# Optimization experiments

Hardware: AMD Instinct MI355X
Metric: run time of the kernel (lower is better)

The kernel has to match this reference:

```python
import jax, jax.numpy as jnp
import numpy as np

N = 16384  # cohort size; original kernel materializes an N x N tril matrix (1 GB fp32)


def setup_inputs() -> dict:
    key = jax.random.key(0)
    k1, k2, k3 = jax.random.split(key, 3)
    pred = jax.random.normal(k1, (N, 1), dtype=jnp.float32)
    # survival times sorted in DESCENDING order (docstring precondition)
    ytime = jnp.sort(jax.random.uniform(k2, (N, 1), dtype=jnp.float32), axis=0)[::-1]
    # binary censoring/event indicator, ~half observed
    yevent = (jax.random.uniform(k3, (N, 1), dtype=jnp.float32) < 0.5).astype(jnp.float32)
    label = jnp.concatenate([ytime, yevent], axis=1)  # [N, 2]
    return {"pred": pred, "label": label}


def reference(pred, label):
    # yevent: [N,1] event indicator (label[:,1]); ytime only fixes ordering/length.
    yevent = label[:, 1:2]
    n_observed = yevent.sum()
    # tril(ones) @ exp(pred) is exactly an inclusive prefix sum over the
    # descending-time-sorted samples: risk_set_sum[i] = sum_{j<=i} exp(pred[j]).
    risk_set_sum = jnp.cumsum(jnp.exp(pred), axis=0)  # [N,1]
    diff = pred - jnp.log(risk_set_sum)               # [N,1]
    sum_diff_in_observed = (diff * yevent).sum()
    cost = jnp.where(n_observed == 0,
                     jnp.float32(0.0),
                     -(sum_diff_in_observed / jnp.maximum(n_observed, 1.0)))
    return cost.reshape(1), n_observed
```

## Files before the change

kernel.cpp:

```cpp
#include <hip/hip_runtime.h>


#define NLL_N     16384
#define NLL_BLOCK 1024
#define NLL_PT    16

__global__ __launch_bounds__(NLL_BLOCK) void nll_kernel(
    const float* __restrict__ pred,
    const float* __restrict__ label,
    float* __restrict__ out)
{
    const int tid  = threadIdx.x;
    const int lane = tid & 63;
    const int wave = tid >> 6;

    float p[NLL_PT];
    const float4* p4 = (const float4*)pred;
    #pragma unroll
    for (int v = 0; v < 4; ++v) {
        float4 x = p4[tid * 4 + v];
        p[v*4+0] = x.x; p[v*4+1] = x.y; p[v*4+2] = x.z; p[v*4+3] = x.w;
    }
    float ev[NLL_PT];
    const float4* l4 = (const float4*)label;
    #pragma unroll
    for (int v = 0; v < 8; ++v) {
        float4 x = l4[tid * 8 + v];
        ev[v*2+0] = x.y;
        ev[v*2+1] = x.w;
    }

    float pref[NLL_PT];
    float run = 0.f;
    #pragma unroll
    for (int i = 0; i < NLL_PT; ++i) { run += __expf(p[i]); pref[i] = run; }

    float inc = run;
    #pragma unroll
    for (int off = 1; off < 64; off <<= 1) {
        float t = __shfl_up(inc, off, 64);
        if (lane >= off) inc += t;
    }
    __shared__ float wsum[16];
    __shared__ float wexc[16];
    if (lane == 63) wsum[wave] = inc;
    __syncthreads();

    if (wave == 0) {
        float x = (lane < 16) ? wsum[lane] : 0.f;
        #pragma unroll
        for (int off = 1; off < 16; off <<= 1) {
            float t = __shfl_up(x, off, 64);
            if (lane >= off) x += t;
        }
        if (lane < 16) wexc[lane] = x - wsum[lane];
    }
    __syncthreads();

    const float base = wexc[wave] + (inc - run);

    float sd = 0.f, se = 0.f;
    #pragma unroll
    for (int i = 0; i < NLL_PT; ++i) {
        float risk = base + pref[i];
        sd = fmaf(ev[i], p[i] - __logf(risk), sd);
        se += ev[i];
    }

    #pragma unroll
    for (int off = 32; off > 0; off >>= 1) {
        sd += __shfl_down(sd, off, 64);
        se += __shfl_down(se, off, 64);
    }
    __shared__ float rd[16], re[16];
    if (lane == 0) { rd[wave] = sd; re[wave] = se; }
    __syncthreads();
    if (tid == 0) {
        float d = 0.f, e = 0.f;
        #pragma unroll
        for (int w = 0; w < 16; ++w) { d += rd[w]; e += re[w]; }
        out[1] = e;
        out[0] = (e == 0.f) ? 0.f : -(d / fmaxf(e, 1.f));
    }
}

extern "C" void kernel_launch(void* const* d_in, const int* in_sizes, int n_in,
                              void* d_out, int out_size, void* d_ws, size_t ws_size,
                              hipStream_t stream) {
    const float* pred  = (const float*)d_in[0];
    const float* label = (const float*)d_in[1];
    float* out = (float*)d_out;
    (void)in_sizes; (void)n_in; (void)out_size; (void)d_ws; (void)ws_size;
    nll_kernel<<<1, NLL_BLOCK, 0, stream>>>(pred, label, out);
}
```

Measured before the change: 61.51 us.

## Split single-block scan into multi-block reduce-then-scan with atomic final reduction

Measured after the change: 62.58 us. About the same (+1.7%).

```diff
diff --git a/kernel.cpp b/kernel.cpp
--- a/kernel.cpp
+++ b/kernel.cpp
@@ -1,86 +1,95 @@
 #include <hip/hip_runtime.h>
 
 
-#define NLL_N     16384
-#define NLL_BLOCK 1024
-#define NLL_PT    16
+#define NLL_N      16384
+#define NLL_CHUNKS 64
+#define NLL_T      256
 
-__global__ __launch_bounds__(NLL_BLOCK) void nll_kernel(
-    const float* __restrict__ pred,
-    const float* __restrict__ label,
-    float* __restrict__ out)
-{
+__global__ __launch_bounds__(NLL_T) void nll_k1(const float* __restrict__ pred,
+                                                float* __restrict__ ws) {
     const int tid  = threadIdx.x;
     const int lane = tid & 63;
     const int wave = tid >> 6;
+    const int i    = blockIdx.x * NLL_T + tid;
 
-    float p[NLL_PT];
-    const float4* p4 = (const float4*)pred;
+    float e = __expf(pred[i]);
     #pragma unroll
-    for (int v = 0; v < 4; ++v) {
-        float4 x = p4[tid * 4 + v];
-        p[v*4+0] = x.x; p[v*4+1] = x.y; p[v*4+2] = x.z; p[v*4+3] = x.w;
-    }
-    float ev[NLL_PT];
-    const float4* l4 = (const float4*)label;
-    #pragma unroll
-    for (int v = 0; v < 8; ++v) {
-        float4 x = l4[tid * 8 + v];
-        ev[v*2+0] = x.y;
-        ev[v*2+1] = x.w;
+    for (int off = 32; off > 0; off >>= 1) e += __shfl_down(e, off, 64);
+
+    __shared__ float s[4];
+    if (lane == 0) s[wave] = e;
+    __syncthreads();
+    if (tid == 0) ws[blockIdx.x] = s[0] + s[1] + s[2] + s[3];
+}
+
+__global__ __launch_bounds__(NLL_T) void nll_k2(const float* __restrict__ pred,
+                                                const float* __restrict__ label,
+                                                float* __restrict__ ws,
+                                                float* __restrict__ out) {
+    const int tid  = threadIdx.x;
+    const int lane = tid & 63;
+    const int wave = tid >> 6;
+    const int blk  = blockIdx.x;
+    const int i    = blk * NLL_T + tid;
+
+    __shared__ float exc[NLL_CHUNKS];
+    __shared__ float wt[4];
+    __shared__ float rd[4], re[4];
+
+    if (wave == 0) {
+        float own = ws[lane];
+        float inc0 = own;
+        #pragma unroll
+        for (int off = 1; off < 64; off <<= 1) {
+            float t = __shfl_up(inc0, off, 64);
+            if (lane >= off) inc0 += t;
+        }
+        exc[lane] = inc0 - own;
     }
 
-    float pref[NLL_PT];
-    float run = 0.f;
-    #pragma unroll
-    for (int i = 0; i < NLL_PT; ++i) { run += __expf(p[i]); pref[i] = run; }
+    float p  = pred[i];
+    float ev = ((const float2*)label)[i].y;
+    float e  = __expf(p);
 
-    float inc = run;
+    float inc = e;
     #pragma unroll
     for (int off = 1; off < 64; off <<= 1) {
         float t = __shfl_up(inc, off, 64);
         if (lane >= off) inc += t;
     }
-    __shared__ float wsum[16];
-    __shared__ float wexc[16];
-    if (lane == 63) wsum[wave] = inc;
+    if (lane == 63) wt[wave] = inc;
     __syncthreads();
 
-    if (wave == 0) {
-        float x = (lane < 16) ? wsum[lane] : 0.f;
-        #pragma unroll
-        for (int off = 1; off < 16; off <<= 1) {
-            float t = __shfl_up(x, off, 64);
-            if (lane >= off) x += t;
-        }
-        if (lane < 16) wexc[lane] = x - wsum[lane];
-    }
-    __syncthreads();
+    float base = exc[blk];
+    #pragma unroll
+    for (int w = 0; w < 4; ++w) if (w < wave) base += wt[w];
 
-    const float base = wexc[wave] + (inc - run);
-
-    float sd = 0.f, se = 0.f;
-    #pragma unroll
-    for (int i = 0; i < NLL_PT; ++i) {
-        float risk = base + pref[i];
-        sd = fmaf(ev[i], p[i] - __logf(risk), sd);
-        se += ev[i];
-    }
+    float risk = base + inc;
+    float sd = ev * (p - __logf(risk));
+    float se = ev;
 
     #pragma unroll
     for (int off = 32; off > 0; off >>= 1) {
         sd += __shfl_down(sd, off, 64);
         se += __shfl_down(se, off, 64);
     }
-    __shared__ float rd[16], re[16];
     if (lane == 0) { rd[wave] = sd; re[wave] = se; }
     __syncthreads();
+
     if (tid == 0) {
-        float d = 0.f, e = 0.f;
-        #pragma unroll
-        for (int w = 0; w < 16; ++w) { d += rd[w]; e += re[w]; }
-        out[1] = e;
-        out[0] = (e == 0.f) ? 0.f : -(d / fmaxf(e, 1.f));
+        float bsd = rd[0] + rd[1] + rd[2] + rd[3];
+        float bse = re[0] + re[1] + re[2] + re[3];
+        atomicAdd(&ws[64], bsd);
+        atomicAdd(&ws[65], bse);
+        __threadfence();
+        unsigned old = atomicAdd((unsigned*)&ws[66], 1u);
+        if (old == NLL_CHUNKS - 1) {
+            __threadfence();
+            float d = atomicAdd(&ws[64], 0.0f);
+            float e2 = atomicAdd(&ws[65], 0.0f);
+            out[1] = e2;
+            out[0] = (e2 == 0.f) ? 0.f : -(d / fmaxf(e2, 1.f));
+        }
     }
 }
 
@@ -90,6 +99,10 @@
     const float* pred  = (const float*)d_in[0];
     const float* label = (const float*)d_in[1];
     float* out = (float*)d_out;
-    (void)in_sizes; (void)n_in; (void)out_size; (void)d_ws; (void)ws_size;
-    nll_kernel<<<1, NLL_BLOCK, 0, stream>>>(pred, label, out);
+    float* ws  = (float*)d_ws;
+    (void)in_sizes; (void)n_in; (void)out_size; (void)ws_size;
+
+    hipMemsetAsync((char*)d_ws + 64 * sizeof(float), 0, 3 * sizeof(float), stream);
+    nll_k1<<<NLL_CHUNKS, NLL_T, 0, stream>>>(pred, ws);
+    nll_k2<<<NLL_CHUNKS, NLL_T, 0, stream>>>(pred, label, ws, out);
 }
```
